# Kernel optimization log

Measured on AMD Instinct MI355X. Metric: run time of the kernel, lower is better.

## Reference

```python
import jax, jax.numpy as jnp
import numpy as np

B, D, H, O, E, R, K, NH = 2048, 512, 2048, 512, 8, 4, 2, 8
DH = O // NH
EPS = 1e-5

def _ln(x, g, b):
    m = x.mean(-1, keepdims=True)
    v = ((x - m) ** 2).mean(-1, keepdims=True)
    return (x - m) / jnp.sqrt(v + EPS) * g + b

def setup_inputs():
    key = jax.random.key(0)
    ks = jax.random.split(key, 16)
    n = lambda k, shape, fan: jax.random.normal(k, shape, jnp.float32) * (fan ** -0.5)
    x = jax.random.normal(ks[0], (B, D), jnp.float32)
    regime = jax.random.randint(ks[1], (B,), 0, R)
    regime_features = jax.nn.one_hot(regime, R, dtype=jnp.float32)
    return dict(
        x=x, regime=regime, regime_features=regime_features,
        ew1=n(ks[2], (R, E, D, H), D), eb1=jnp.zeros((R, E, H)),
        lng=jnp.ones((R, E, H)), lnb=jnp.zeros((R, E, H)),
        ew2=n(ks[3], (R, E, H, O), H), eb2=jnp.zeros((R, E, O)),
        rw1=n(ks[4], (R, D + R, H), D + R), rb1=jnp.zeros((R, H)),
        rw2=n(ks[5], (R, H, E), H), rb2=jnp.zeros((R, E)),
        ipw=n(ks[6], (3 * O, O), O), ipb=jnp.zeros((3 * O,)),
        opw=n(ks[7], (O, O), O), opb=jnp.zeros((O,)),
        ang=jnp.ones((O,)), anb=jnp.zeros((O,)),
    )

def _forward(x, regime, regime_features, ew1, eb1, lng, lnb, ew2, eb2, rw1, rb1, rw2, rb2, ipw, ipb, opw, opb, ang, anb):
    B_ = x.shape[0]
    bi = jnp.arange(B_)
    # regime-conditioned routing: compute logits for all regimes densely, select per sample
    ri = jnp.concatenate([x, regime_features], axis=-1)                  # [B, D+R]
    rh = jax.nn.relu(jnp.einsum('bf,rfh->rbh', ri, rw1) + rb1[:, None])
    logits = (jnp.einsum('rbh,rhe->rbe', rh, rw2) + rb2[:, None])[regime, bi]  # [B, E]
    w = jax.nn.softmax(logits, axis=-1)
    tkw, tki = jax.lax.top_k(w, K)
    tkw = tkw / tkw.sum(-1, keepdims=True)
    # experts: all regimes x all experts, then select the per-sample regime block
    h = jnp.einsum('bd,redh->rebh', x, ew1) + eb1[:, :, None]            # [R, E, B, H]
    h = jax.nn.relu(_ln(h, lng[:, :, None], lnb[:, :, None]))
    eo = jnp.einsum('rebh,reho->rebo', h, ew2) + eb2[:, :, None] + x[None, None]  # identity residual (D == O)
    eo = eo.transpose(0, 2, 1, 3)[regime, bi]                            # [B, E, O]
    # group attention over expert axis (torch MultiheadAttention, eval mode)
    qkv = eo @ ipw.T + ipb
    q, k, v = jnp.split(qkv, 3, axis=-1)
    sh = lambda t: t.reshape(B_, E, NH, DH).transpose(0, 2, 1, 3)
    q, k, v = sh(q), sh(k), sh(v)
    attn = jax.nn.softmax(jnp.einsum('bhqd,bhkd->bhqk', q, k) / np.sqrt(DH).astype(np.float32), axis=-1)
    av = jnp.einsum('bhqk,bhkd->bhqd', attn, v).transpose(0, 2, 1, 3).reshape(B_, E, O)
    eo = _ln(eo + av @ opw.T + opb, ang, anb)
    # top-k combine
    gathered = jnp.take_along_axis(eo, tki[:, :, None], axis=1)          # [B, K, O]
    return jnp.sum(tkw[:, :, None] * gathered, axis=1)

def reference(x, regime, regime_features, ew1, eb1, lng, lnb, ew2, eb2, rw1, rb1, rw2, rb2, ipw, ipb, opw, opb, ang, anb):
    return _forward(x, regime, regime_features, ew1, eb1, lng, lnb, ew2, eb2, rw1, rb1, rw2, rb2, ipw, ipb, opw, opb, ang, anb)
```

## Files before the change

### kernel.cpp

```cpp
#include <hip/hip_runtime.h>
#include <hip/hip_bf16.h>
#include <cstddef>

typedef __attribute__((ext_vector_type(8))) short short8;
typedef __attribute__((ext_vector_type(4))) float f32x4;

constexpr int CB = 2048;
constexpr int CD = 512;
constexpr int CH = 2048;
constexpr int CO = 512;
constexpr int CE = 8;
constexpr int CR = 4;

__device__ __forceinline__ float bs2f(short s){
  union { float f; unsigned u; } u; u.u = ((unsigned)(unsigned short)s) << 16; return u.f;
}
__device__ __forceinline__ short f2bs(float x){
  union { __hip_bfloat16 h; short s; } u; u.h = __float2bfloat16(x); return u.s;
}

#define GLL(g, l) __builtin_amdgcn_global_load_lds((const __attribute__((address_space(1))) void*)(g), (__attribute__((address_space(3))) void*)(l), 16, 0, 0)

__device__ __forceinline__ short8 ln8(short8 raw, float mean, float rstd,
                                      float4 g01, float4 g23, float4 b01, float4 b23){
  const float g[8] = {g01.x,g01.y,g01.z,g01.w,g23.x,g23.y,g23.z,g23.w};
  const float b[8] = {b01.x,b01.y,b01.z,b01.w,b23.x,b23.y,b23.z,b23.w};
  short8 o;
#pragma unroll
  for (int j = 0; j < 8; j++){
    const float v = (bs2f(raw[j]) - mean) * rstd * g[j] + b[j];
    o[j] = f2bs(fmaxf(v, 0.f));
  }
  return o;
}

__device__ __forceinline__ void block_reduce2(float& a, float& b){
#pragma unroll
  for (int off = 32; off; off >>= 1){ a += __shfl_xor(a, off, 64); b += __shfl_xor(b, off, 64); }
  __shared__ float sa[4], sb[4];
  const int wid = threadIdx.x >> 6, lane = threadIdx.x & 63;
  __syncthreads();
  if (lane == 0){ sa[wid] = a; sb[wid] = b; }
  __syncthreads();
  a = sa[0] + sa[1] + sa[2] + sa[3];
  b = sb[0] + sb[1] + sb[2] + sb[3];
}

__global__ void k_count(const int* __restrict__ regime, int* __restrict__ meta){
  int b = blockIdx.x * 256 + threadIdx.x;
  if (b < CB) atomicAdd(&meta[8 + regime[b]], 1);
}
__global__ void k_scan(int* meta){
  if (threadIdx.x == 0){
    int c0 = meta[8], c1 = meta[9], c2 = meta[10], c3 = meta[11];
    meta[0] = 0; meta[1] = c0; meta[2] = c0 + c1; meta[3] = c0 + c1 + c2; meta[4] = c0 + c1 + c2 + c3;
  }
}
__global__ void k_scatter(const int* __restrict__ regime, int* __restrict__ meta, int* __restrict__ perm){
  int b = blockIdx.x * 256 + threadIdx.x;
  if (b < CB){
    int r = regime[b];
    int pos = atomicAdd(&meta[12 + r], 1);
    perm[meta[r] + pos] = b;
  }
}

__global__ __launch_bounds__(256) void k_xsplit(const float* __restrict__ x, const int* __restrict__ perm,
                                                short* __restrict__ xp, short* __restrict__ xd){
  const int i = blockIdx.x;
  const int b = perm[i];
  const int c = threadIdx.x * 2;
  float2 v = *(const float2*)(x + (size_t)b * CD + c);
  short2 hi; hi.x = f2bs(v.x); hi.y = f2bs(v.y);
  short2 lo; lo.x = f2bs(v.x - bs2f(hi.x)); lo.y = f2bs(v.y - bs2f(hi.y));
  *(short2*)(xp + (size_t)i * CD + c) = hi;
  short* row = xd + (size_t)i * 1536;
  *(short2*)(row + c) = hi;
  *(short2*)(row + 512 + c) = hi;
  *(short2*)(row + 1024 + c) = lo;
}

__global__ __launch_bounds__(256) void k_cvt2(const float* __restrict__ a, short* __restrict__ ao, int na,
                                              const float* __restrict__ b, short* __restrict__ bo, int nb){
  int i = (blockIdx.x * 256 + threadIdx.x) * 8;
  const float* src; short* dst;
  if (i < na){ src = a + i; dst = ao + i; }
  else { int j = i - na; if (j >= nb) return; src = b + j; dst = bo + j; }
  float4 u = *(const float4*)(src);
  float4 v = *(const float4*)(src + 4);
  short8 o;
  o[0]=f2bs(u.x); o[1]=f2bs(u.y); o[2]=f2bs(u.z); o[3]=f2bs(u.w);
  o[4]=f2bs(v.x); o[5]=f2bs(v.y); o[6]=f2bs(v.z); o[7]=f2bs(v.w);
  *(short8*)(dst) = o;
}

__global__ __launch_bounds__(256) void k_cvt_t(const float* __restrict__ in, short* __restrict__ outp, int K, int N){
  __shared__ float tile[64][65];
  const int z = blockIdx.z;
  const int k0 = blockIdx.y * 64, n0 = blockIdx.x * 64;
  const float* src = in + (size_t)z * K * N;
  short* dst = outp + (size_t)z * K * N;
  const int t = threadIdx.x;
  const int kk = t >> 4, nq = (t & 15) * 4;
#pragma unroll
  for (int j = 0; j < 4; j++){
    float4 v = *(const float4*)(src + (size_t)(k0 + kk + j * 16) * N + n0 + nq);
    tile[kk + j * 16][nq] = v.x; tile[kk + j * 16][nq + 1] = v.y;
    tile[kk + j * 16][nq + 2] = v.z; tile[kk + j * 16][nq + 3] = v.w;
  }
  __syncthreads();
  const int n = t >> 2, kq = (t & 3) * 16;
  short8 o0, o1;
#pragma unroll
  for (int j = 0; j < 8; j++) o0[j] = f2bs(tile[kq + j][n]);
#pragma unroll
  for (int j = 0; j < 8; j++) o1[j] = f2bs(tile[kq + 8 + j][n]);
  short* drow = dst + (size_t)(n0 + n) * K + k0 + kq;
  *(short8*)(drow) = o0;
  *(short8*)(drow + 8) = o1;
}

__global__ __launch_bounds__(256) void k_rwt(const float* __restrict__ rw1, const float* __restrict__ rb1,
                                             short* __restrict__ Bp, float* __restrict__ rbias){
  __shared__ float tile[64][65];
  const int r = blockIdx.z;
  const int k0 = blockIdx.y * 64, n0 = blockIdx.x * 64;
  const float* src = rw1 + (size_t)r * (CD + CR) * CH;
  short* dst = Bp + (size_t)r * CH * 1536;
  const int t = threadIdx.x;
  if (blockIdx.y == 0 && t < 64){
    const int n = n0 + t;
    rbias[r * CH + n] = rb1[(size_t)r * CH + n] + src[((size_t)(CD + r)) * CH + n];
  }
  const int kk = t >> 4, nq = (t & 15) * 4;
#pragma unroll
  for (int j = 0; j < 4; j++){
    float4 v = *(const float4*)(src + (size_t)(k0 + kk + j * 16) * CH + n0 + nq);
    tile[kk + j * 16][nq] = v.x; tile[kk + j * 16][nq + 1] = v.y;
    tile[kk + j * 16][nq + 2] = v.z; tile[kk + j * 16][nq + 3] = v.w;
  }
  __syncthreads();
  const int n = t >> 2, kq = (t & 3) * 16;
  short8 h0, h1, l0, l1;
#pragma unroll
  for (int j = 0; j < 8; j++){
    float f = tile[kq + j][n];
    short h = f2bs(f); h0[j] = h; l0[j] = f2bs(f - bs2f(h));
  }
#pragma unroll
  for (int j = 0; j < 8; j++){
    float f = tile[kq + 8 + j][n];
    short h = f2bs(f); h1[j] = h; l1[j] = f2bs(f - bs2f(h));
  }
  short* drow = dst + (size_t)(n0 + n) * 1536;
  *(short8*)(drow + k0 + kq) = h0;        *(short8*)(drow + k0 + kq + 8) = h1;
  *(short8*)(drow + 512 + k0 + kq) = l0;  *(short8*)(drow + 512 + k0 + kq + 8) = l1;
  *(short8*)(drow + 1024 + k0 + kq) = h0; *(short8*)(drow + 1024 + k0 + kq + 8) = h1;
}

__global__ __launch_bounds__(256) void k_logits2(
    const float* __restrict__ part, const float* __restrict__ rb2,
    const int* __restrict__ meta, const int* __restrict__ perm,
    int* __restrict__ tki, float* __restrict__ tkw, int* __restrict__ qrows){
  const int wid = threadIdx.x >> 6, lane = threadIdx.x & 63;
  const int i = blockIdx.x * 4 + wid;
  const int r = (i >= meta[1]) + (i >= meta[2]) + (i >= meta[3]);
  const int p0 = lane >> 3, e = lane & 7;
  float v = 0.f;
#pragma unroll
  for (int j = 0; j < 4; j++)
    v += part[((size_t)(p0 + 8 * j) * CB + i) * 8 + e];
  v += __shfl_xor(v, 8, 64);
  v += __shfl_xor(v, 16, 64);
  v += __shfl_xor(v, 32, 64);
  v += rb2[r * CE + e];
  float l8[8];
#pragma unroll
  for (int e2 = 0; e2 < 8; e2++) l8[e2] = __shfl(v, e2, 64);
  if (lane == 0){
    int i1 = 0; float m1 = l8[0];
#pragma unroll
    for (int e2 = 1; e2 < 8; e2++) if (l8[e2] > m1){ m1 = l8[e2]; i1 = e2; }
    int i2 = -1; float m2 = -1e30f;
#pragma unroll
    for (int e2 = 0; e2 < 8; e2++) if (e2 != i1 && l8[e2] > m2){ m2 = l8[e2]; i2 = e2; }
    const float e2w = __expf(m2 - m1);
    const float w1 = 1.f / (1.f + e2w);
    const int b = perm[i];
    tki[b * 2] = i1; tki[b * 2 + 1] = i2;
    tkw[b * 2] = w1; tkw[b * 2 + 1] = e2w * w1;
    qrows[b * 2] = b * CE + i1; qrows[b * 2 + 1] = b * CE + i2;
  }
}

template<int EPI, bool SWZ>
__global__ __launch_bounds__(256) void gemm_bf16(
    const short* __restrict__ A, long lda,
    const short* __restrict__ Wt, long ldw,
    const int* __restrict__ goff, int fixedM, int Ksub, int N,
    const float* __restrict__ bias, long bstride,
    short* __restrict__ outb, float* __restrict__ outf,
    const int* __restrict__ operm, const float* __restrict__ xtra,
    int mbs, int nbs, float* __restrict__ pstat){
  constexpr int BK = 32;
  __shared__ __align__(16) short lds[2][8192];

  int bx, by, bz;
  if constexpr (SWZ){
    const int s = blockIdx.x;
    const int chunk = gridDim.x >> 3;
    const int l = (s & 7) * chunk + (s >> 3);
    bx = l % nbs; const int t2 = l / nbs; by = t2 % mbs; bz = t2 / mbs;
  } else { bx = blockIdx.x; by = blockIdx.y; bz = blockIdx.z; }

  const int z = bz;
  int g0 = 0, Mg = fixedM;
  if (goff){ const int r = (EPI == 6) ? z : (z >> 3); g0 = goff[r]; Mg = goff[r + 1] - g0; }
  const int m0 = by * 128;
  if (m0 >= Mg) return;
  const int n0 = bx * 128;
  const int e = z & 7;

  const short* Ab;
  if constexpr (EPI == 1 || EPI == 6) Ab = A + (size_t)g0 * (size_t)lda;
  else Ab = A;
  const short* Wb = Wt + (size_t)z * (size_t)N * (size_t)ldw;

  const int tid = threadIdx.x;
  const int lane = tid & 63, wid = tid >> 6;
  const int srow = lane >> 2;
  const int sc = (((lane & 3) ^ ((srow >> 1) & 3)) << 3);

  int ar0 = m0 + wid * 32 + srow;
  int ar1 = ar0 + 16;
  if (ar0 > Mg - 1) ar0 = Mg - 1;
  if (ar1 > Mg - 1) ar1 = Mg - 1;
  if constexpr (EPI == 3){
    if (operm){ ar0 = operm[ar0]; ar1 = operm[ar1]; }
  }
  const short* ga0 = Ab + (size_t)ar0 * lda + sc;
  const short* ga1 = Ab + (size_t)ar1 * lda + sc;
  const int brow = n0 + wid * 32 + srow;
  const short* gb0 = Wb + (size_t)brow * ldw + sc;
  const short* gb1 = gb0 + (size_t)16 * ldw;

  const int wm = (wid >> 1) * 64, wn = (wid & 1) * 64;
  const int r16 = lane & 15, kb = lane >> 4;
  const int rsw = (r16 >> 1) & 3;

  f32x4 acc[4][4];
#pragma unroll
  for (int a = 0; a < 4; a++)
#pragma unroll
    for (int b = 0; b < 4; b++) acc[a][b] = (f32x4){0.f, 0.f, 0.f, 0.f};

  const int NT = Ksub / BK;
  int buf = 0;

  {
    short* dA = &lds[0][0] + wid * 1024;
    short* dB = &lds[0][4096] + wid * 1024;
    GLL(ga0, dA); GLL(ga1, dA + 512);
    GLL(gb0, dB); GLL(gb1, dB + 512);
  }
  __syncthreads();

  for (int t = 0; t < NT; ++t){
    if (t + 1 < NT){
      const int kof = (t + 1) * BK;
      short* dA = &lds[buf ^ 1][0] + wid * 1024;
      short* dB = &lds[buf ^ 1][4096] + wid * 1024;
      GLL(ga0 + kof, dA); GLL(ga1 + kof, dA + 512);
      GLL(gb0 + kof, dB); GLL(gb1 + kof, dB + 512);
    }
    const short* sA = &lds[buf][0];
    const short* sB = &lds[buf][4096];
    short8 af[4], bfv[4];
#pragma unroll
    for (int mi = 0; mi < 4; mi++)
      af[mi] = *(const short8*)(sA + (wm + mi * 16 + r16) * 32 + ((kb ^ rsw) << 3));
#pragma unroll
    for (int ni = 0; ni < 4; ni++)
      bfv[ni] = *(const short8*)(sB + (wn + ni * 16 + r16) * 32 + ((kb ^ rsw) << 3));
#pragma unroll
    for (int mi = 0; mi < 4; mi++)
#pragma unroll
      for (int ni = 0; ni < 4; ni++)
        acc[mi][ni] = __builtin_amdgcn_mfma_f32_16x16x32_bf16(af[mi], bfv[ni], acc[mi][ni], 0, 0, 0);
    __syncthreads();
    buf ^= 1;
  }

  if constexpr (EPI == 1){
    const int slot = bx * 2 + (wid & 1);
#pragma unroll
    for (int mi = 0; mi < 4; mi++){
#pragma unroll
      for (int q = 0; q < 4; q++){
        const int i = m0 + wm + mi * 16 + kb * 4 + q;
        float vv[4]; float sv = 0.f, sq = 0.f;
#pragma unroll
        for (int ni = 0; ni < 4; ni++){
          const int n = n0 + wn + ni * 16 + r16;
          const float v = acc[mi][ni][q] + bias[(size_t)z * bstride + n];
          vv[ni] = v; sv += v; sq += v * v;
        }
#pragma unroll
        for (int off = 1; off < 16; off <<= 1){
          sv += __shfl_xor(sv, off, 64);
          sq += __shfl_xor(sq, off, 64);
        }
        if (i < Mg){
#pragma unroll
          for (int ni = 0; ni < 4; ni++){
            const int n = n0 + wn + ni * 16 + r16;
            outb[((size_t)e * CB + (g0 + i)) * (size_t)N + n] = f2bs(vv[ni]);
          }
          if (r16 == 0){
            float* sp = pstat + ((size_t)slot * (CE * CB) + (size_t)e * CB + (g0 + i)) * 2;
            sp[0] = sv; sp[1] = sq;
          }
        }
      }
    }
    return;
  }

  if constexpr (EPI == 6){
    const int hbase = n0 + wn;
    float wv[4][8]; float rbv[4];
#pragma unroll
    for (int ni = 0; ni < 4; ni++){
      const int h = hbase + ni * 16 + r16;
      rbv[ni] = bias[(size_t)z * CH + h];
      const float* wp = xtra + ((size_t)z * CH + h) * 8;
#pragma unroll
      for (int e2 = 0; e2 < 8; e2++) wv[ni][e2] = wp[e2];
    }
    const int slot = bx * 2 + (wid & 1);
#pragma unroll
    for (int mi = 0; mi < 4; mi++){
#pragma unroll
      for (int q = 0; q < 4; q++){
        float tmp[8];
#pragma unroll
        for (int e2 = 0; e2 < 8; e2++) tmp[e2] = 0.f;
#pragma unroll
        for (int ni = 0; ni < 4; ni++){
          const float v = fmaxf(acc[mi][ni][q] + rbv[ni], 0.f);
#pragma unroll
          for (int e2 = 0; e2 < 8; e2++) tmp[e2] += v * wv[ni][e2];
        }
#pragma unroll
        for (int e2 = 0; e2 < 8; e2++){
          tmp[e2] += __shfl_xor(tmp[e2], 1, 64);
          tmp[e2] += __shfl_xor(tmp[e2], 2, 64);
          tmp[e2] += __shfl_xor(tmp[e2], 4, 64);
          tmp[e2] += __shfl_xor(tmp[e2], 8, 64);
        }
        const int row = wm + mi * 16 + kb * 4 + q;
        if (r16 == 0 && m0 + row < Mg){
          float* dp = outf + ((size_t)slot * CB + (g0 + m0 + row)) * 8;
#pragma unroll
          for (int e2 = 0; e2 < 8; e2++) dp[e2] = tmp[e2];
        }
      }
    }
    return;
  }

#pragma unroll
  for (int mi = 0; mi < 4; mi++){
#pragma unroll
    for (int q = 0; q < 4; q++){
      const int i = m0 + wm + mi * 16 + kb * 4 + q;
      if (i >= Mg) continue;
#pragma unroll
      for (int ni = 0; ni < 4; ni++){
        const int n = n0 + wn + ni * 16 + r16;
        float v = acc[mi][ni][q] + bias[n];
        if constexpr (EPI == 3){
          outb[(size_t)i * (size_t)N + n] = f2bs(v);
        } else {
          outf[(size_t)i * (size_t)N + n] = v;
        }
      }
    }
  }
}

__global__ __launch_bounds__(256) void gemm2_ln(
    const short* __restrict__ hact, const short* __restrict__ Wt,
    const int* __restrict__ goff, const float* __restrict__ pstat,
    const float* __restrict__ lng, const float* __restrict__ lnb,
    short* __restrict__ P, long pstr, const int* __restrict__ operm){
  constexpr int BK = 32, KS = 1024;
  __shared__ __align__(16) short lds[2][8192];
  __shared__ float smean[128], srstd[128];

  const int s = blockIdx.x;
  const int chunk = gridDim.x >> 3;
  const int l = (s & 7) * chunk + (s >> 3);
  const int bx = l & 3; const int t2 = l >> 2; const int by = t2 & 15; const int bz = t2 >> 4;
  const int ks = bz & 1, z = bz >> 1;
  const int r = z >> 3, e = z & 7;
  const int g0 = goff[r], Mg = goff[r + 1] - g0;
  const int m0 = by * 128;
  if (m0 >= Mg) return;
  const int n0 = bx * 128;
  const long kbase = (long)ks * KS;

  const int tid = threadIdx.x, lane = tid & 63, wid = tid >> 6;

  if (tid < 128){
    int lr = m0 + tid; if (lr > Mg - 1) lr = Mg - 1;
    const size_t rid = (size_t)e * CB + g0 + lr;
    float S = 0.f, Q = 0.f;
#pragma unroll
    for (int p = 0; p < 32; p++){
      const float2 pp = *(const float2*)(pstat + ((size_t)p * (CE * CB) + rid) * 2);
      S += pp.x; Q += pp.y;
    }
    const float mean = S * (1.f / CH);
    const float var = Q * (1.f / CH) - mean * mean;
    smean[tid] = mean;
    srstd[tid] = rsqrtf(fmaxf(var, 0.f) + 1e-5f);
  }

  const int srow = lane >> 2;
  const int c = lane & 3;
  const int dsw = (srow >> 1) & 3;

  const int lr0 = wid * 32 + srow, lr1 = lr0 + 16;
  const int cr0 = (m0 + lr0 > Mg - 1) ? (Mg - 1 - m0) : lr0;
  const int cr1 = (m0 + lr1 > Mg - 1) ? (Mg - 1 - m0) : lr1;

  const short* ga0 = hact + ((size_t)e * CB + g0 + (m0 + cr0)) * (size_t)CH + kbase + c * 8;
  const short* ga1 = hact + ((size_t)e * CB + g0 + (m0 + cr1)) * (size_t)CH + kbase + c * 8;
  const float* gp = lng + (size_t)(r * CE + e) * CH + kbase + c * 8;
  const float* bp = lnb + (size_t)(r * CE + e) * CH + kbase + c * 8;

  const short* Wb = Wt + (size_t)z * (size_t)CO * (size_t)CH;
  const int brow = n0 + wid * 32 + srow;
  const int scB = ((c ^ dsw) << 3);
  const short* gb0 = Wb + (size_t)brow * CH + kbase + scB;
  const short* gb1 = gb0 + (size_t)16 * CH;

  const int wof0 = lr0 * 32 + ((c ^ dsw) << 3);
  const int wof1 = lr1 * 32 + ((c ^ dsw) << 3);

  __syncthreads();
  const float mean0 = smean[cr0], rstd0 = srstd[cr0];
  const float mean1 = smean[cr1], rstd1 = srstd[cr1];

  const int wm = (wid >> 1) * 64, wn = (wid & 1) * 64;
  const int r16 = lane & 15, kb = lane >> 4;
  const int rsw = (r16 >> 1) & 3;

  f32x4 acc[4][4];
#pragma unroll
  for (int a = 0; a < 4; a++)
#pragma unroll
    for (int b = 0; b < 4; b++) acc[a][b] = (f32x4){0.f, 0.f, 0.f, 0.f};

  const int NT = KS / BK;
  int buf = 0;

  {
    short8 a0 = *(const short8*)(ga0);
    short8 a1 = *(const short8*)(ga1);
    float4 g01 = *(const float4*)(gp), g23 = *(const float4*)(gp + 4);
    float4 b01 = *(const float4*)(bp), b23 = *(const float4*)(bp + 4);
    short* dB = &lds[0][4096] + wid * 1024;
    GLL(gb0, dB); GLL(gb1, dB + 512);
    *(short8*)(&lds[0][0] + wof0) = ln8(a0, mean0, rstd0, g01, g23, b01, b23);
    *(short8*)(&lds[0][0] + wof1) = ln8(a1, mean1, rstd1, g01, g23, b01, b23);
  }
  __syncthreads();

  for (int t = 0; t < NT; ++t){
    short8 na0, na1; float4 ng01, ng23, nb01, nb23;
    if (t + 1 < NT){
      const int kof = (t + 1) * BK;
      na0 = *(const short8*)(ga0 + kof);
      na1 = *(const short8*)(ga1 + kof);
      ng01 = *(const float4*)(gp + kof); ng23 = *(const float4*)(gp + kof + 4);
      nb01 = *(const float4*)(bp + kof); nb23 = *(const float4*)(bp + kof + 4);
      short* dB = &lds[buf ^ 1][4096] + wid * 1024;
      GLL(gb0 + kof, dB); GLL(gb1 + kof, dB + 512);
    }
    const short* sA = &lds[buf][0];
    const short* sB = &lds[buf][4096];
    short8 af[4], bfv[4];
#pragma unroll
    for (int mi = 0; mi < 4; mi++)
      af[mi] = *(const short8*)(sA + (wm + mi * 16 + r16) * 32 + ((kb ^ rsw) << 3));
#pragma unroll
    for (int ni = 0; ni < 4; ni++)
      bfv[ni] = *(const short8*)(sB + (wn + ni * 16 + r16) * 32 + ((kb ^ rsw) << 3));
#pragma unroll
    for (int mi = 0; mi < 4; mi++)
#pragma unroll
      for (int ni = 0; ni < 4; ni++)
        acc[mi][ni] = __builtin_amdgcn_mfma_f32_16x16x32_bf16(af[mi], bfv[ni], acc[mi][ni], 0, 0, 0);
    if (t + 1 < NT){
      *(short8*)(&lds[buf ^ 1][0] + wof0) = ln8(na0, mean0, rstd0, ng01, ng23, nb01, nb23);
      *(short8*)(&lds[buf ^ 1][0] + wof1) = ln8(na1, mean1, rstd1, ng01, ng23, nb01, nb23);
    }
    __syncthreads();
    buf ^= 1;
  }

#pragma unroll
  for (int mi = 0; mi < 4; mi++){
#pragma unroll
    for (int q = 0; q < 4; q++){
      const int i = m0 + wm + mi * 16 + kb * 4 + q;
      if (i >= Mg) continue;
      const int borig = operm[g0 + i];
#pragma unroll
      for (int ni = 0; ni < 4; ni++){
        const int n = n0 + wn + ni * 16 + r16;
        P[(size_t)ks * pstr + ((size_t)borig * CE + e) * (size_t)CO + n] = f2bs(acc[mi][ni][q]);
      }
    }
  }
}

__global__ __launch_bounds__(256) void k_eo(const short* __restrict__ P, long pstr,
    const float* __restrict__ eb2, const float* __restrict__ x, const int* __restrict__ regime,
    short* __restrict__ eo){
  const int b = blockIdx.x, e = blockIdx.y;
  const int r = regime[b];
  const int c = threadIdx.x * 2;
  const size_t idx = (((size_t)b * CE + e) << 9) + c;
  short2 a0 = *(const short2*)(P + idx);
  short2 a1 = *(const short2*)(P + pstr + idx);
  float2 xr = *(const float2*)(x + (size_t)b * CD + c);
  float2 eb = *(const float2*)(eb2 + (((size_t)r * CE + e) << 9) + c);
  short2 o;
  o.x = f2bs(bs2f(a0.x) + bs2f(a1.x) + xr.x + eb.x);
  o.y = f2bs(bs2f(a0.y) + bs2f(a1.y) + xr.y + eb.y);
  *(short2*)(eo + idx) = o;
}

__global__ __launch_bounds__(128) void k_attn(const short* __restrict__ qb, const short* __restrict__ kv,
    const int* __restrict__ tki, short* __restrict__ av){
  const int b = blockIdx.x;
  const int j = threadIdx.x >> 6, d = threadIdx.x & 63;
  const short* q = qb + (size_t)(b * 2 + j) * CO;
  const short* base = kv + (size_t)b * CE * 1024;
#pragma unroll
  for (int h = 0; h < 8; h++){
    const float qv = bs2f(q[h * 64 + d]);
    float sc[8];
#pragma unroll
    for (int e = 0; e < 8; e++){
      float pp = qv * bs2f(base[(size_t)e * 1024 + h * 64 + d]);
#pragma unroll
      for (int off = 32; off; off >>= 1) pp += __shfl_xor(pp, off, 64);
      sc[e] = pp * 0.125f;
    }
    float m = sc[0];
#pragma unroll
    for (int e = 1; e < 8; e++) m = fmaxf(m, sc[e]);
    float den = 0.f, avd = 0.f;
#pragma unroll
    for (int e = 0; e < 8; e++){
      const float pe = __expf(sc[e] - m);
      den += pe;
      avd += pe * bs2f(base[(size_t)e * 1024 + 512 + h * 64 + d]);
    }
    av[((size_t)b * 2 + j) * CO + h * 64 + d] = f2bs(avd / den);
  }
}

__global__ __launch_bounds__(256) void k_final(const short* __restrict__ eo,
    const float* __restrict__ proj, const int* __restrict__ tki, const float* __restrict__ tkw,
    const float* __restrict__ ang, const float* __restrict__ anb, float* __restrict__ out){
  const int b = blockIdx.x, t = threadIdx.x;
  float o0 = 0.f, o1 = 0.f;
#pragma unroll
  for (int j = 0; j < 2; j++){
    const int s = tki[b * 2 + j];
    const float w = tkw[b * 2 + j];
    const short* ep = eo + ((size_t)b * CE + s) * CO;
    const float* pp = proj + ((size_t)b * 2 + j) * CO;
    const float v0 = bs2f(ep[t]) + pp[t];
    const float v1 = bs2f(ep[t + 256]) + pp[t + 256];
    float sm = v0 + v1, sq = v0 * v0 + v1 * v1;
    block_reduce2(sm, sq);
    const float mean = sm * (1.f / CO);
    const float rstd = rsqrtf(fmaxf(sq * (1.f / CO) - mean * mean, 0.f) + 1e-5f);
    o0 += w * ((v0 - mean) * rstd * ang[t] + anb[t]);
    o1 += w * ((v1 - mean) * rstd * ang[t + 256] + anb[t + 256]);
  }
  out[(size_t)b * CO + t] = o0;
  out[(size_t)b * CO + t + 256] = o1;
}

extern "C" void kernel_launch(void* const* d_in, const int* in_sizes, int n_in,
                              void* d_out, int out_size, void* d_ws, size_t ws_size,
                              hipStream_t stream){
  const float* x    = (const float*)d_in[0];
  const int*   regime = (const int*)d_in[1];
  const float* ew1  = (const float*)d_in[3];
  const float* eb1  = (const float*)d_in[4];
  const float* lng  = (const float*)d_in[5];
  const float* lnb  = (const float*)d_in[6];
  const float* ew2  = (const float*)d_in[7];
  const float* eb2  = (const float*)d_in[8];
  const float* rw1  = (const float*)d_in[9];
  const float* rb1  = (const float*)d_in[10];
  const float* rw2  = (const float*)d_in[11];
  const float* rb2  = (const float*)d_in[12];
  const float* ipw  = (const float*)d_in[13];
  const float* ipb  = (const float*)d_in[14];
  const float* opw  = (const float*)d_in[15];
  const float* opb  = (const float*)d_in[16];
  const float* ang  = (const float*)d_in[17];
  const float* anb  = (const float*)d_in[18];
  float* out = (float*)d_out;

  char* ws = (char*)d_ws;
  int*   meta  = (int*)(ws);
  int*   perm  = (int*)(ws + (16u << 10));
  int*   tki   = (int*)(ws + (32u << 10));
  float* tkw   = (float*)(ws + (48u << 10));
  int*   qrows = (int*)(ws + (64u << 10));
  float* rbias = (float*)(ws + (80u << 10));
  short* ipwb  = (short*)(ws + (256u << 10));
  short* opwb  = (short*)(ws + (1792u << 10));
  short* xp    = (short*)(ws + (2304u << 10));
  short* eo    = (short*)(ws + (4352u << 10));
  short* hact  = (short*)(ws + (22ull << 20));
  short* qkv   = (short*)(ws + (22ull << 20));
  short* qb    = (short*)(ws + (54ull << 20));
  short* av    = (short*)(ws + (58ull << 20));
  float* proj  = (float*)(ws + (62ull << 20));
  float* part  = (float*)(ws + (70ull << 20));
  short* wt    = (short*)(ws + (86ull << 20));
  short* P     = (short*)(ws + (150ull << 20));
  short* xd    = (short*)(ws + (216ull << 20));
  float* pstat = (float*)(ws + (224ull << 20));
  const long PSTR = (long)CB * CE * CO;

  hipMemsetAsync(meta, 0, 1024, stream);
  k_count  <<<8, 256, 0, stream>>>(regime, meta);
  k_scan   <<<1, 64, 0, stream>>>(meta);
  k_scatter<<<8, 256, 0, stream>>>(regime, meta, perm);
  k_xsplit <<<CB, 256, 0, stream>>>(x, perm, xp, xd);
  k_cvt2   <<<512, 256, 0, stream>>>(ipw, ipwb, 1536 * 512, opw, opwb, 512 * 512);

  k_rwt<<<dim3(32, 8, CR), 256, 0, stream>>>(rw1, rb1, wt, rbias);
  gemm_bf16<6, false><<<dim3(16, 16, CR), 256, 0, stream>>>(
      xd, 1536, wt, 1536, meta, 0, 1536, CH, rbias, 0,
      nullptr, part, nullptr, rw2, 0, 0, nullptr);
  k_logits2<<<CB / 4, 256, 0, stream>>>(part, rb2, meta, perm, tki, tkw, qrows);

  k_cvt_t<<<dim3(32, 8, 32), 256, 0, stream>>>(ew1, wt, CD, CH);
  gemm_bf16<1, true><<<8192, 256, 0, stream>>>(
      xp, CD, wt, CD, meta, 0, CD, CH, eb1, CH, hact, nullptr, nullptr, nullptr, 16, 16, pstat);

  k_cvt_t<<<dim3(8, 32, 32), 256, 0, stream>>>(ew2, wt, CH, CO);
  gemm2_ln<<<4096, 256, 0, stream>>>(hact, wt, meta, pstat, lng, lnb, P, PSTR, perm);
  k_eo<<<dim3(CB, CE), 256, 0, stream>>>(P, PSTR, eb2, x, regime, eo);

  gemm_bf16<3, true><<<1024, 256, 0, stream>>>(
      eo, CO, ipwb + (size_t)512 * 512, CO, nullptr, CB * CE, CO, 1024, ipb + 512, 0,
      qkv, nullptr, nullptr, nullptr, 128, 8, nullptr);
  gemm_bf16<3, false><<<dim3(4, 32, 1), 256, 0, stream>>>(
      eo, CO, ipwb, CO, nullptr, CB * 2, CO, CO, ipb, 0,
      qb, nullptr, qrows, nullptr, 0, 0, nullptr);

  k_attn<<<CB, 128, 0, stream>>>(qb, qkv, tki, av);

  gemm_bf16<4, false><<<dim3(4, 32, 1), 256, 0, stream>>>(
      av, CO, opwb, CO, nullptr, CB * 2, CO, CO, opb, 0,
      nullptr, proj, nullptr, nullptr, 0, 0, nullptr);

  k_final<<<CB, 256, 0, stream>>>(eo, proj, tki, tkw, ang, anb, out);
  (void)in_sizes; (void)n_in; (void)out_size; (void)ws_size;
}
```

Baseline: 448.7 us.

## Merge prep, routing and GEMM launches into fewer fused multi-role kernels

Replaces the count/scan/scatter kernels with a single-block shared-memory bucketing kernel. All input conversions and weight transposes now run in one large prep kernel, and the weights get separate buffers so they no longer share a workspace slot. Independent GEMMs (expert GEMM1 with the router GEMM, and the K/V with the Q projection) run in combined launches that dispatch on block index. The goal is to cut launch overhead and the GPU going idle between small kernels. The cost is larger workspace use and possibly higher register or LDS pressure from the combined bodies.

```diff
diff --git a/kernel.cpp b/kernel.cpp
--- a/kernel.cpp
+++ b/kernel.cpp
@@ -46,60 +46,33 @@
   b = sb[0] + sb[1] + sb[2] + sb[3];
 }
 
-__global__ void k_count(const int* __restrict__ regime, int* __restrict__ meta){
-  int b = blockIdx.x * 256 + threadIdx.x;
-  if (b < CB) atomicAdd(&meta[8 + regime[b]], 1);
-}
-__global__ void k_scan(int* meta){
-  if (threadIdx.x == 0){
-    int c0 = meta[8], c1 = meta[9], c2 = meta[10], c3 = meta[11];
+__global__ __launch_bounds__(1024) void k_bucket(const int* __restrict__ regime,
+                                                 int* __restrict__ meta, int* __restrict__ perm){
+  __shared__ int cnt[4], cur[4];
+  const int t = threadIdx.x;
+  if (t < 4) cnt[t] = 0;
+  __syncthreads();
+  const int r0 = regime[t];
+  const int r1 = regime[t + 1024];
+  atomicAdd(&cnt[r0], 1);
+  atomicAdd(&cnt[r1], 1);
+  __syncthreads();
+  if (t == 0){
+    const int c0 = cnt[0], c1 = cnt[1], c2 = cnt[2], c3 = cnt[3];
     meta[0] = 0; meta[1] = c0; meta[2] = c0 + c1; meta[3] = c0 + c1 + c2; meta[4] = c0 + c1 + c2 + c3;
-  }
-}
-__global__ void k_scatter(const int* __restrict__ regime, int* __restrict__ meta, int* __restrict__ perm){
-  int b = blockIdx.x * 256 + threadIdx.x;
-  if (b < CB){
-    int r = regime[b];
-    int pos = atomicAdd(&meta[12 + r], 1);
-    perm[meta[r] + pos] = b;
-  }
-}
-
-__global__ __launch_bounds__(256) void k_xsplit(const float* __restrict__ x, const int* __restrict__ perm,
-                                                short* __restrict__ xp, short* __restrict__ xd){
-  const int i = blockIdx.x;
-  const int b = perm[i];
-  const int c = threadIdx.x * 2;
-  float2 v = *(const float2*)(x + (size_t)b * CD + c);
-  short2 hi; hi.x = f2bs(v.x); hi.y = f2bs(v.y);
-  short2 lo; lo.x = f2bs(v.x - bs2f(hi.x)); lo.y = f2bs(v.y - bs2f(hi.y));
-  *(short2*)(xp + (size_t)i * CD + c) = hi;
-  short* row = xd + (size_t)i * 1536;
-  *(short2*)(row + c) = hi;
-  *(short2*)(row + 512 + c) = hi;
-  *(short2*)(row + 1024 + c) = lo;
-}
-
-__global__ __launch_bounds__(256) void k_cvt2(const float* __restrict__ a, short* __restrict__ ao, int na,
-                                              const float* __restrict__ b, short* __restrict__ bo, int nb){
-  int i = (blockIdx.x * 256 + threadIdx.x) * 8;
-  const float* src; short* dst;
-  if (i < na){ src = a + i; dst = ao + i; }
-  else { int j = i - na; if (j >= nb) return; src = b + j; dst = bo + j; }
-  float4 u = *(const float4*)(src);
-  float4 v = *(const float4*)(src + 4);
-  short8 o;
-  o[0]=f2bs(u.x); o[1]=f2bs(u.y); o[2]=f2bs(u.z); o[3]=f2bs(u.w);
-  o[4]=f2bs(v.x); o[5]=f2bs(v.y); o[6]=f2bs(v.z); o[7]=f2bs(v.w);
-  *(short8*)(dst) = o;
-}
-
-__global__ __launch_bounds__(256) void k_cvt_t(const float* __restrict__ in, short* __restrict__ outp, int K, int N){
-  __shared__ float tile[64][65];
-  const int z = blockIdx.z;
-  const int k0 = blockIdx.y * 64, n0 = blockIdx.x * 64;
-  const float* src = in + (size_t)z * K * N;
-  short* dst = outp + (size_t)z * K * N;
+    cur[0] = 0; cur[1] = c0; cur[2] = c0 + c1; cur[3] = c0 + c1 + c2;
+  }
+  __syncthreads();
+  { int p = atomicAdd(&cur[r0], 1); perm[p] = t; }
+  { int p = atomicAdd(&cur[r1], 1); perm[p] = t + 1024; }
+}
+
+__device__ __forceinline__ void cvtt_tile(float (*tile)[65], const float* __restrict__ in,
+                                          short* __restrict__ outp, int K, int N,
+                                          int bx, int by, int bz){
+  const int k0 = by * 64, n0 = bx * 64;
+  const float* src = in + (size_t)bz * K * N;
+  short* dst = outp + (size_t)bz * K * N;
   const int t = threadIdx.x;
   const int kk = t >> 4, nq = (t & 15) * 4;
 #pragma unroll
@@ -120,42 +93,89 @@
   *(short8*)(drow + 8) = o1;
 }
 
-__global__ __launch_bounds__(256) void k_rwt(const float* __restrict__ rw1, const float* __restrict__ rb1,
-                                             short* __restrict__ Bp, float* __restrict__ rbias){
+__global__ __launch_bounds__(256) void k_prep(
+    const float* __restrict__ x, const int* __restrict__ perm,
+    short* __restrict__ xp, short* __restrict__ xd,
+    const float* __restrict__ ipw, short* __restrict__ ipwb,
+    const float* __restrict__ opw, short* __restrict__ opwb,
+    const float* __restrict__ rw1, const float* __restrict__ rb1,
+    short* __restrict__ wtR, float* __restrict__ rbias,
+    const float* __restrict__ ew1, short* __restrict__ wt1,
+    const float* __restrict__ ew2, short* __restrict__ wt2){
   __shared__ float tile[64][65];
-  const int r = blockIdx.z;
-  const int k0 = blockIdx.y * 64, n0 = blockIdx.x * 64;
-  const float* src = rw1 + (size_t)r * (CD + CR) * CH;
-  short* dst = Bp + (size_t)r * CH * 1536;
+  const int s = blockIdx.x;
   const int t = threadIdx.x;
-  if (blockIdx.y == 0 && t < 64){
-    const int n = n0 + t;
-    rbias[r * CH + n] = rb1[(size_t)r * CH + n] + src[((size_t)(CD + r)) * CH + n];
-  }
-  const int kk = t >> 4, nq = (t & 15) * 4;
-#pragma unroll
-  for (int j = 0; j < 4; j++){
-    float4 v = *(const float4*)(src + (size_t)(k0 + kk + j * 16) * CH + n0 + nq);
-    tile[kk + j * 16][nq] = v.x; tile[kk + j * 16][nq + 1] = v.y;
-    tile[kk + j * 16][nq + 2] = v.z; tile[kk + j * 16][nq + 3] = v.w;
-  }
-  __syncthreads();
-  const int n = t >> 2, kq = (t & 3) * 16;
-  short8 h0, h1, l0, l1;
-#pragma unroll
-  for (int j = 0; j < 8; j++){
-    float f = tile[kq + j][n];
-    short h = f2bs(f); h0[j] = h; l0[j] = f2bs(f - bs2f(h));
-  }
-#pragma unroll
-  for (int j = 0; j < 8; j++){
-    float f = tile[kq + 8 + j][n];
-    short h = f2bs(f); h1[j] = h; l1[j] = f2bs(f - bs2f(h));
-  }
-  short* drow = dst + (size_t)(n0 + n) * 1536;
-  *(short8*)(drow + k0 + kq) = h0;        *(short8*)(drow + k0 + kq + 8) = h1;
-  *(short8*)(drow + 512 + k0 + kq) = l0;  *(short8*)(drow + 512 + k0 + kq + 8) = l1;
-  *(short8*)(drow + 1024 + k0 + kq) = h0; *(short8*)(drow + 1024 + k0 + kq + 8) = h1;
+  if (s < 2048){
+    const int i = s, b = perm[i], c = t * 2;
+    float2 v = *(const float2*)(x + (size_t)b * CD + c);
+    short2 hi; hi.x = f2bs(v.x); hi.y = f2bs(v.y);
+    short2 lo; lo.x = f2bs(v.x - bs2f(hi.x)); lo.y = f2bs(v.y - bs2f(hi.y));
+    *(short2*)(xp + (size_t)i * CD + c) = hi;
+    short* row = xd + (size_t)i * 1536;
+    *(short2*)(row + c) = hi;
+    *(short2*)(row + 512 + c) = hi;
+    *(short2*)(row + 1024 + c) = lo;
+    return;
+  }
+  if (s < 2560){
+    int i = ((s - 2048) * 256 + t) * 8;
+    const int na = 1536 * 512, nb = 512 * 512;
+    const float* src; short* dst;
+    if (i < na){ src = ipw + i; dst = ipwb + i; }
+    else { int j = i - na; if (j >= nb) return; src = opw + j; dst = opwb + j; }
+    float4 u = *(const float4*)(src);
+    float4 v = *(const float4*)(src + 4);
+    short8 o;
+    o[0]=f2bs(u.x); o[1]=f2bs(u.y); o[2]=f2bs(u.z); o[3]=f2bs(u.w);
+    o[4]=f2bs(v.x); o[5]=f2bs(v.y); o[6]=f2bs(v.z); o[7]=f2bs(v.w);
+    *(short8*)(dst) = o;
+    return;
+  }
+  if (s < 3584){
+    const int i = s - 2560;
+    const int bx = i & 31, by = (i >> 5) & 7, r = i >> 8;
+    const int k0 = by * 64, n0 = bx * 64;
+    const float* src = rw1 + (size_t)r * (CD + CR) * CH;
+    short* dst = wtR + (size_t)r * CH * 1536;
+    if (by == 0 && t < 64){
+      const int n = n0 + t;
+      rbias[r * CH + n] = rb1[(size_t)r * CH + n] + src[((size_t)(CD + r)) * CH + n];
+    }
+    const int kk = t >> 4, nq = (t & 15) * 4;
+#pragma unroll
+    for (int j = 0; j < 4; j++){
+      float4 v = *(const float4*)(src + (size_t)(k0 + kk + j * 16) * CH + n0 + nq);
+      tile[kk + j * 16][nq] = v.x; tile[kk + j * 16][nq + 1] = v.y;
+      tile[kk + j * 16][nq + 2] = v.z; tile[kk + j * 16][nq + 3] = v.w;
+    }
+    __syncthreads();
+    const int n = t >> 2, kq = (t & 3) * 16;
+    short8 h0, h1, l0, l1;
+#pragma unroll
+    for (int j = 0; j < 8; j++){
+      float f = tile[kq + j][n];
+      short h = f2bs(f); h0[j] = h; l0[j] = f2bs(f - bs2f(h));
+    }
+#pragma unroll
+    for (int j = 0; j < 8; j++){
+      float f = tile[kq + 8 + j][n];
+      short h = f2bs(f); h1[j] = h; l1[j] = f2bs(f - bs2f(h));
+    }
+    short* drow = dst + (size_t)(n0 + n) * 1536;
+    *(short8*)(drow + k0 + kq) = h0;        *(short8*)(drow + k0 + kq + 8) = h1;
+    *(short8*)(drow + 512 + k0 + kq) = l0;  *(short8*)(drow + 512 + k0 + kq + 8) = l1;
+    *(short8*)(drow + 1024 + k0 + kq) = h0; *(short8*)(drow + 1024 + k0 + kq + 8) = h1;
+    return;
+  }
+  if (s < 11776){
+    const int i = s - 3584;
+    cvtt_tile(tile, ew1, wt1, CD, CH, i & 31, (i >> 5) & 7, i >> 8);
+    return;
+  }
+  {
+    const int i = s - 11776;
+    cvtt_tile(tile, ew2, wt2, CH, CO, i & 7, (i >> 3) & 31, i >> 8);
+  }
 }
 
 __global__ __launch_bounds__(256) void k_logits2(
@@ -193,25 +213,18 @@
   }
 }
 
-template<int EPI, bool SWZ>
-__global__ __launch_bounds__(256) void gemm_bf16(
+template<int EPI>
+__device__ __forceinline__ void gemm_body(
+    int bx, int by, int bz,
     const short* __restrict__ A, long lda,
     const short* __restrict__ Wt, long ldw,
     const int* __restrict__ goff, int fixedM, int Ksub, int N,
     const float* __restrict__ bias, long bstride,
     short* __restrict__ outb, float* __restrict__ outf,
     const int* __restrict__ operm, const float* __restrict__ xtra,
-    int mbs, int nbs, float* __restrict__ pstat){
+    float* __restrict__ pstat){
   constexpr int BK = 32;
   __shared__ __align__(16) short lds[2][8192];
-
-  int bx, by, bz;
-  if constexpr (SWZ){
-    const int s = blockIdx.x;
-    const int chunk = gridDim.x >> 3;
-    const int l = (s & 7) * chunk + (s >> 3);
-    bx = l % nbs; const int t2 = l / nbs; by = t2 % mbs; bz = t2 / mbs;
-  } else { bx = blockIdx.x; by = blockIdx.y; bz = blockIdx.z; }
 
   const int z = bz;
   int g0 = 0, Mg = fixedM;
@@ -387,6 +400,49 @@
       }
     }
   }
+}
+
+__global__ __launch_bounds__(256) void k_rg1(
+    const short* __restrict__ xp, const short* __restrict__ wt1, const int* __restrict__ meta,
+    const float* __restrict__ eb1, short* __restrict__ hact, float* __restrict__ pstat,
+    const short* __restrict__ xd, const short* __restrict__ wtR,
+    const float* __restrict__ rbias, const float* __restrict__ rw2, float* __restrict__ part){
+  const int s = blockIdx.x;
+  if (s < 8192){
+    const int chunk = 1024;
+    const int l = (s & 7) * chunk + (s >> 3);
+    const int bx = l % 16; const int t2 = l / 16; const int by = t2 % 16; const int bz = t2 / 16;
+    gemm_body<1>(bx, by, bz, xp, CD, wt1, CD, meta, 0, CD, CH, eb1, CH,
+                 hact, nullptr, nullptr, nullptr, pstat);
+  } else {
+    const int i = s - 8192;
+    gemm_body<6>(i & 15, (i >> 4) & 15, i >> 8, xd, 1536, wtR, 1536, meta, 0, 1536, CH,
+                 rbias, 0, nullptr, part, nullptr, rw2, nullptr);
+  }
+}
+
+__global__ __launch_bounds__(256) void k_kvq(
+    const short* __restrict__ eo, const short* __restrict__ ipwb, const float* __restrict__ ipb,
+    short* __restrict__ qkv, short* __restrict__ qb, const int* __restrict__ qrows){
+  const int s = blockIdx.x;
+  if (s < 1024){
+    const int chunk = 128;
+    const int l = (s & 7) * chunk + (s >> 3);
+    const int bx = l % 8, by = l / 8;
+    gemm_body<3>(bx, by, 0, eo, CO, ipwb + (size_t)512 * 512, CO, nullptr, CB * CE, CO, 1024,
+                 ipb + 512, 0, qkv, nullptr, nullptr, nullptr, nullptr);
+  } else {
+    const int i = s - 1024;
+    gemm_body<3>(i & 3, i >> 2, 0, eo, CO, ipwb, CO, nullptr, CB * 2, CO, CO,
+                 ipb, 0, qb, nullptr, qrows, nullptr, nullptr);
+  }
+}
+
+__global__ __launch_bounds__(256) void k_proj(
+    const short* __restrict__ av, const short* __restrict__ opwb, const float* __restrict__ opb,
+    float* __restrict__ proj){
+  gemm_body<4>(blockIdx.x, blockIdx.y, 0, av, CO, opwb, CO, nullptr, CB * 2, CO, CO,
+               opb, 0, nullptr, proj, nullptr, nullptr, nullptr);
 }
 
 __global__ __launch_bounds__(256) void gemm2_ln(
@@ -638,47 +694,26 @@
   short* qb    = (short*)(ws + (54ull << 20));
   short* av    = (short*)(ws + (58ull << 20));
   float* proj  = (float*)(ws + (62ull << 20));
-  float* part  = (float*)(ws + (70ull << 20));
-  short* wt    = (short*)(ws + (86ull << 20));
-  short* P     = (short*)(ws + (150ull << 20));
-  short* xd    = (short*)(ws + (216ull << 20));
-  float* pstat = (float*)(ws + (224ull << 20));
+  short* wtR   = (short*)(ws + (88ull << 20));
+  short* wt1   = (short*)(ws + (112ull << 20));
+  short* wt2   = (short*)(ws + (176ull << 20));
+  short* P     = (short*)(ws + (240ull << 20));
+  short* xd    = (short*)(ws + (272ull << 20));
+  float* pstat = (float*)(ws + (280ull << 20));
+  float* part  = (float*)(ws + (286ull << 20));
   const long PSTR = (long)CB * CE * CO;
 
-  hipMemsetAsync(meta, 0, 1024, stream);
-  k_count  <<<8, 256, 0, stream>>>(regime, meta);
-  k_scan   <<<1, 64, 0, stream>>>(meta);
-  k_scatter<<<8, 256, 0, stream>>>(regime, meta, perm);
-  k_xsplit <<<CB, 256, 0, stream>>>(x, perm, xp, xd);
-  k_cvt2   <<<512, 256, 0, stream>>>(ipw, ipwb, 1536 * 512, opw, opwb, 512 * 512);
-
-  k_rwt<<<dim3(32, 8, CR), 256, 0, stream>>>(rw1, rb1, wt, rbias);
-  gemm_bf16<6, false><<<dim3(16, 16, CR), 256, 0, stream>>>(
-      xd, 1536, wt, 1536, meta, 0, 1536, CH, rbias, 0,
-      nullptr, part, nullptr, rw2, 0, 0, nullptr);
+  k_bucket<<<1, 1024, 0, stream>>>(regime, meta, perm);
+  k_prep<<<19968, 256, 0, stream>>>(x, perm, xp, xd, ipw, ipwb, opw, opwb,
+                                    rw1, rb1, wtR, rbias, ew1, wt1, ew2, wt2);
+  k_rg1<<<8192 + 1024, 256, 0, stream>>>(xp, wt1, meta, eb1, hact, pstat,
+                                         xd, wtR, rbias, rw2, part);
   k_logits2<<<CB / 4, 256, 0, stream>>>(part, rb2, meta, perm, tki, tkw, qrows);
-
-  k_cvt_t<<<dim3(32, 8, 32), 256, 0, stream>>>(ew1, wt, CD, CH);
-  gemm_bf16<1, true><<<8192, 256, 0, stream>>>(
-      xp, CD, wt, CD, meta, 0, CD, CH, eb1, CH, hact, nullptr, nullptr, nullptr, 16, 16, pstat);
-
-  k_cvt_t<<<dim3(8, 32, 32), 256, 0, stream>>>(ew2, wt, CH, CO);
-  gemm2_ln<<<4096, 256, 0, stream>>>(hact, wt, meta, pstat, lng, lnb, P, PSTR, perm);
+  gemm2_ln<<<4096, 256, 0, stream>>>(hact, wt2, meta, pstat, lng, lnb, P, PSTR, perm);
   k_eo<<<dim3(CB, CE), 256, 0, stream>>>(P, PSTR, eb2, x, regime, eo);
-
-  gemm_bf16<3, true><<<1024, 256, 0, stream>>>(
-      eo, CO, ipwb + (size_t)512 * 512, CO, nullptr, CB * CE, CO, 1024, ipb + 512, 0,
-      qkv, nullptr, nullptr, nullptr, 128, 8, nullptr);
-  gemm_bf16<3, false><<<dim3(4, 32, 1), 256, 0, stream>>>(
-      eo, CO, ipwb, CO, nullptr, CB * 2, CO, CO, ipb, 0,
-      qb, nullptr, qrows, nullptr, 0, 0, nullptr);
-
+  k_kvq<<<1024 + 128, 256, 0, stream>>>(eo, ipwb, ipb, qkv, qb, qrows);
   k_attn<<<CB, 128, 0, stream>>>(qb, qkv, tki, av);
-
-  gemm_bf16<4, false><<<dim3(4, 32, 1), 256, 0, stream>>>(
-      av, CO, opwb, CO, nullptr, CB * 2, CO, CO, opb, 0,
-      nullptr, proj, nullptr, nullptr, 0, 0, nullptr);
-
+  k_proj<<<dim3(4, 32), 256, 0, stream>>>(av, opwb, opb, proj);
   k_final<<<CB, 256, 0, stream>>>(eo, proj, tki, tkw, ang, anb, out);
   (void)in_sizes; (void)n_in; (void)out_size; (void)ws_size;
 }
```

Measured after the change: 427.4 us. 4.7% less time.
